# Performance work log

Hardware: AMD Instinct MI355X
Metric: run time of the kernel (lower is better)

## Reference

```python
import jax, jax.numpy as jnp
import numpy as np


def setup_inputs() -> dict:
    key = jax.random.key(0)
    ks = jax.random.split(key, 4)
    B, T, D, U = 64, 512, 1024, 1024
    scale = 1.0 / np.sqrt(D)
    return {
        "x": jax.random.normal(ks[0], (B, T, D), dtype=jnp.float32),
        "kernel_z": jax.random.normal(ks[1], (D, U), dtype=jnp.float32) * scale,
        "kernel_r": jax.random.normal(ks[2], (D, U), dtype=jnp.float32) * scale,
        "kernel_h": jax.random.normal(ks[3], (D, U), dtype=jnp.float32) * scale,
        "memory_z": jnp.ones((U,), dtype=jnp.float32),
        "memory_r": jnp.ones((U,), dtype=jnp.float32),
        "bias_z": jnp.zeros((U,), dtype=jnp.float32),
        "bias_r": jnp.zeros((U,), dtype=jnp.float32),
        "bias_h": jnp.zeros((U,), dtype=jnp.float32),
    }


def _bru_scan(x, kernel_z, kernel_r, kernel_h, memory_z, memory_r,
              bias_z, bias_r, bias_h):
    B, T, D = x.shape
    U = kernel_z.shape[1]
    # Precompute the three input projections for all timesteps at once
    # (same math as per-step K.dot; hoisted out of the recurrence).
    xz = jnp.einsum('btd,du->btu', x, kernel_z) + bias_z  # [B,T,U]
    xr = jnp.einsum('btd,du->btu', x, kernel_r) + bias_r
    xh = jnp.einsum('btd,du->btu', x, kernel_h) + bias_h

    def step(h, xs):
        xz_t, xr_t, xh_t = xs
        r = jnp.tanh(xr_t + h * memory_r) + 1.0
        z = jax.nn.sigmoid(xz_t + h * memory_z)
        hh = jnp.tanh(xh_t + r * h)
        out = (1.0 - z) * hh + z * h
        return out, out

    h0 = jnp.zeros((B, U), dtype=x.dtype)
    # scan over time axis
    xs = (jnp.swapaxes(xz, 0, 1), jnp.swapaxes(xr, 0, 1), jnp.swapaxes(xh, 0, 1))
    _, outs = jax.lax.scan(step, h0, xs)  # outs: [T,B,U]
    return jnp.swapaxes(outs, 0, 1)  # [B,T,U]


def reference(x, kernel_z, kernel_r, kernel_h, memory_z, memory_r,
              bias_z, bias_r, bias_h):
    return _bru_scan(x, kernel_z, kernel_r, kernel_h, memory_z, memory_r,
                     bias_z, bias_r, bias_h)
```

## Files before the change

kernel.cpp:

```cpp
#include <hip/hip_runtime.h>
#include <cmath>

using f16x8 = __attribute__((ext_vector_type(8))) _Float16;
using f32x4 = __attribute__((ext_vector_type(4))) float;

__device__ __forceinline__ void gld16(void* lds, const void* g) {
    __builtin_amdgcn_global_load_lds(
        (const __attribute__((address_space(1))) unsigned int*)g,
        (__attribute__((address_space(3))) unsigned int*)lds, 16, 0, 0);
}


__global__ __launch_bounds__(256)
void bru_conv_a(const float* __restrict__ x, char* __restrict__ Ablob,
                int T, int D, int Tc, int t0, int Mc)
{
    const int gid = blockIdx.x * 256 + threadIdx.x;
    const int kt = gid / Mc;
    const int m  = gid - kt * Mc;
    const int mt = m >> 7, row = m & 127;

    const long xrow = (long)(m / Tc) * T + t0 + (m % Tc);
    const float* src = x + xrow * (long)D + kt * 32;

    float v[32];
    #pragma unroll
    for (int i = 0; i < 8; ++i)
        *(float4*)&v[i * 4] = *(const float4*)(src + i * 4);

    _Float16 hi[32], lo[32];
    #pragma unroll
    for (int k = 0; k < 32; ++k) {
        hi[k] = (_Float16)v[k];
        lo[k] = (_Float16)(v[k] - (float)hi[k]);
    }

    char* base = Ablob + ((size_t)(mt * 34 + kt)) * 16384 + (size_t)row * 128;
    #pragma unroll
    for (int q = 0; q < 4; ++q) {
        _Float16 oh[8], ol[8];
        #pragma unroll
        for (int j = 0; j < 8; ++j) { oh[j] = hi[q * 8 + j]; ol[j] = lo[q * 8 + j]; }
        *(f16x8*)(base + (((q    ) ^ (row & 7)) << 4)) = *(f16x8*)oh;
        *(f16x8*)(base + (((q + 4) ^ (row & 7)) << 4)) = *(f16x8*)ol;
    }
}

__global__ __launch_bounds__(256)
void bru_conv_w(const float* __restrict__ wz, const float* __restrict__ wr,
                const float* __restrict__ wh, char* __restrict__ Wblob,
                int D, int U)
{
    const int gid  = blockIdx.x * 256 + threadIdx.x;
    const int blob = gid >> 8;
    const int row  = gid & 255;

    const int g    = blob >> 7;
    const int rest = blob & 127;
    const int nt   = rest >> 5;
    const int kt   = rest & 31;

    const float* W = (g == 0) ? wz : (g == 1) ? wr : wh;
    const int ucol = nt * 256 + row;

    char* base = Wblob + ((size_t)((g * 4 + nt) * 34 + kt)) * 16384 + (size_t)row * 64;
    #pragma unroll
    for (int q = 0; q < 4; ++q) {
        _Float16 o[8];
        #pragma unroll
        for (int j = 0; j < 8; ++j)
            o[j] = (_Float16)W[(long)(kt * 32 + q * 8 + j) * U + ucol];
        *(f16x8*)(base + ((q ^ ((row >> 1) & 3)) << 4)) = *(f16x8*)o;
    }
}

__global__ __launch_bounds__(256, 2)
void bru_gemm_mfma(const char* __restrict__ Ablob, const char* __restrict__ Wblob,
                   const float* __restrict__ bz, const float* __restrict__ br,
                   const float* __restrict__ bh,
                   _Float16* __restrict__ proj,
                   int nmt, int U, int Mc)
{
    __shared__ char sm[65536];

    const int ngrid = gridDim.x;
    const int bid   = blockIdx.x;
    int lid = bid;
    if ((ngrid & 7) == 0) lid = (bid & 7) * (ngrid >> 3) + (bid >> 3);
    const int mt  = lid / 12;
    const int rem = lid - mt * 12;
    const int g   = rem >> 2;
    const int nt  = rem & 3;

    const int tid  = threadIdx.x;
    const int lane = tid & 63;
    const int w    = tid >> 6;
    const int wm   = w >> 1, wn = w & 1;
    const int l15  = lane & 15;
    const int lgrp = lane >> 4;

    const char* asrc = Ablob + (size_t)(mt * 34) * 16384;
    const char* bsrc = Wblob + (size_t)((g * 4 + nt) * 34) * 16384;
    const int st = tid * 16;

    const int abase = (wm * 64 + l15) * 128;
    const int slotA = (lgrp ^ (l15 & 7)) << 4;
    const int bbase = 32768 + (wn * 128 + l15) * 64;
    const int slotB = (lgrp ^ ((l15 >> 1) & 3)) << 4;

    f32x4 acc[4][8];
    #pragma unroll
    for (int i = 0; i < 4; ++i)
        #pragma unroll
        for (int j = 0; j < 8; ++j) acc[i][j] = (f32x4)0.f;

#define STAGE(kt_) do { \
    const int bb_ = (kt_) & 1; \
    _Pragma("unroll") for (int c_ = 0; c_ < 4; ++c_) \
        gld16(sm + bb_ * 16384 + c_ * 4096 + st, \
              asrc + (size_t)(kt_) * 16384 + c_ * 4096 + st); \
    _Pragma("unroll") for (int c_ = 0; c_ < 4; ++c_) \
        gld16(sm + 32768 + bb_ * 16384 + c_ * 4096 + st, \
              bsrc + (size_t)(kt_) * 16384 + c_ * 4096 + st); } while (0)

    STAGE(0);
    __syncthreads();

    for (int kt = 0; kt < 32; ++kt) {
        STAGE(kt + 1);

        const char* sa = sm + (kt & 1) * 16384;
        const char* sb = sm + (kt & 1) * 16384;

        f16x8 bf[8];
        #pragma unroll
        for (int j = 0; j < 8; ++j)
            bf[j] = *(const f16x8*)(sb + bbase + j * 1024 + slotB);
        #pragma unroll
        for (int f = 0; f < 4; ++f) {
            f16x8 ah = *(const f16x8*)(sa + abase + f * 2048 + slotA);
            f16x8 al = *(const f16x8*)(sa + abase + f * 2048 + (slotA ^ 64));
            #pragma unroll
            for (int j = 0; j < 8; ++j) {
                acc[f][j] = __builtin_amdgcn_mfma_f32_16x16x32_f16(ah, bf[j], acc[f][j], 0, 0, 0);
                acc[f][j] = __builtin_amdgcn_mfma_f32_16x16x32_f16(al, bf[j], acc[f][j], 0, 0, 0);
            }
        }

        __syncthreads();
    }
#undef STAGE

    const float* bias = (g == 0) ? bz : (g == 1) ? br : bh;
    const int n0 = nt * 256 + wn * 128;
    float bcol[8];
    #pragma unroll
    for (int j = 0; j < 8; ++j) bcol[j] = bias[n0 + j * 16 + l15];

    _Float16* cbase = proj + (size_t)g * Mc * U + (size_t)n0 + l15;
    #pragma unroll
    for (int f = 0; f < 4; ++f) {
        #pragma unroll
        for (int reg = 0; reg < 4; ++reg) {
            const int row = mt * 128 + wm * 64 + f * 16 + lgrp * 4 + reg;
            #pragma unroll
            for (int j = 0; j < 8; ++j)
                cbase[(size_t)row * U + j * 16] = (_Float16)(acc[f][j][reg] + bcol[j]);
        }
    }
}

#define PF 8
__global__ __launch_bounds__(256)
void bru_scan(const _Float16* __restrict__ proj,
              const float* __restrict__ mz, const float* __restrict__ mr,
              float* __restrict__ out,
              float* __restrict__ hstate,
              int B, int T, int U, int Tc, int t0, int Mc)
{
    const int idx = blockIdx.x * blockDim.x + threadIdx.x;
    const int b = idx / U;
    const int u = idx - b * U;

    float h = (t0 == 0) ? 0.f : hstate[idx];
    const float vmz = mz[u];
    const float vmr = mr[u];

    const _Float16* pz = proj + (long)b * Tc * U + u;
    const _Float16* pr = pz + (long)Mc * U;
    const _Float16* ph = pr + (long)Mc * U;
    float* po = out + ((long)b * T + t0) * U + u;

    _Float16 fz[PF], fr[PF], fh[PF];
    #pragma unroll
    for (int i = 0; i < PF; ++i) {
        const long o = (long)((i < Tc) ? i : (Tc - 1)) * U;
        fz[i] = pz[o]; fr[i] = pr[o]; fh[i] = ph[o];
    }

    for (int t = 0; t < Tc; t += PF) {
        #pragma unroll
        for (int i = 0; i < PF; ++i) {
            const float xz = (float)fz[i];
            const float xr = (float)fr[i];
            const float xh = (float)fh[i];
            {
                int tn = t + i + PF; if (tn > Tc - 1) tn = Tc - 1;
                const long o = (long)tn * U;
                fz[i] = pz[o]; fr[i] = pr[o]; fh[i] = ph[o];
            }
            const float e2r = __expf(2.f * (xr + h * vmr));
            const float rr  = 2.f - 2.f / (e2r + 1.f);
            const float zz  = 1.f / (1.f + __expf(-(xz + h * vmz)));
            const float e2h = __expf(2.f * (xh + rr * h));
            const float hh  = 1.f - 2.f / (e2h + 1.f);
            h = (1.f - zz) * hh + zz * h;
            if (t + i < Tc) po[(long)(t + i) * U] = h;
        }
    }
    hstate[idx] = h;
}

extern "C" void kernel_launch(void* const* d_in, const int* in_sizes, int n_in,
                              void* d_out, int out_size, void* d_ws, size_t ws_size,
                              hipStream_t stream)
{
    const float* x  = (const float*)d_in[0];
    const float* wz = (const float*)d_in[1];
    const float* wr = (const float*)d_in[2];
    const float* wh = (const float*)d_in[3];
    const float* mz = (const float*)d_in[4];
    const float* mr = (const float*)d_in[5];
    const float* bz = (const float*)d_in[6];
    const float* br = (const float*)d_in[7];
    const float* bh = (const float*)d_in[8];

    const int B = 64, T = 512, D = 1024, U = 1024;

    const size_t h_bytes = (size_t)B * U * sizeof(float);
    const size_t w_bytes = (size_t)12 * 34 * 16384;

    int Tc = T;
    while (Tc > 4) {
        const int nmt_ = B * Tc / 128;
        const size_t a_bytes_ = (size_t)nmt_ * 34 * 16384;
        const size_t p_bytes_ = 3ull * B * Tc * U * sizeof(_Float16);
        if (h_bytes + w_bytes + a_bytes_ + p_bytes_ <= ws_size) break;
        Tc >>= 1;
    }
    const int nmt = B * Tc / 128;
    const int Mc  = B * Tc;
    const size_t a_bytes = (size_t)nmt * 34 * 16384;

    float*    h_state = (float*)d_ws;
    char*     Wblob   = (char*)d_ws + h_bytes;
    char*     Ablob   = (char*)d_ws + h_bytes + w_bytes;
    _Float16* proj    = (_Float16*)((char*)d_ws + h_bytes + w_bytes + a_bytes);

    bru_conv_w<<<12 * 32 * 256 / 256, 256, 0, stream>>>(wz, wr, wh, Wblob, D, U);

    for (int t0 = 0; t0 < T; t0 += Tc) {
        bru_conv_a<<<(Mc * 32) / 256, 256, 0, stream>>>(x, Ablob, T, D, Tc, t0, Mc);

        bru_gemm_mfma<<<3 * nmt * 4, 256, 0, stream>>>(
            Ablob, Wblob, bz, br, bh, proj, nmt, U, Mc);

        bru_scan<<<(B * U) / 256, 256, 0, stream>>>(
            proj, mz, mr, (float*)d_out, h_state, B, T, U, Tc, t0, Mc);
    }
}
```

Before: 541.9 us.

## Load GEMM B operand directly from global into registers, halve LDS

The weight matrix is repacked into an MFMA-fragment-ordered layout so each lane fetches its B fragments straight from global/L2 into registers, double-buffered across k-steps. LDS use drops to 32KB and holds only the A tiles, which removes the LDS staging and reads for B. In exchange each block issues many more global loads per k-step, since B is no longer shared through LDS, and keeps 16 extra vector registers live, which may hurt occupancy or latency hiding. The weight conversion kernel is rewritten to emit the new layout.

Result: no change. 543.0 us (+0.2%).

```diff
diff --git a/kernel.cpp b/kernel.cpp
--- a/kernel.cpp
+++ b/kernel.cpp
@@ -51,27 +51,20 @@
                 const float* __restrict__ wh, char* __restrict__ Wblob,
                 int D, int U)
 {
-    const int gid  = blockIdx.x * 256 + threadIdx.x;
-    const int blob = gid >> 8;
-    const int row  = gid & 255;
-
-    const int g    = blob >> 7;
-    const int rest = blob & 127;
-    const int nt   = rest >> 5;
-    const int kt   = rest & 31;
+    const int gid = blockIdx.x * 256 + threadIdx.x;
+    const int g    = gid >> 17;
+    const int rest = gid & 131071;
+    const int qg   = rest >> 10;
+    const int u    = rest & 1023;
 
     const float* W = (g == 0) ? wz : (g == 1) ? wr : wh;
-    const int ucol = nt * 256 + row;
-
-    char* base = Wblob + ((size_t)((g * 4 + nt) * 34 + kt)) * 16384 + (size_t)row * 64;
-    #pragma unroll
-    for (int q = 0; q < 4; ++q) {
-        _Float16 o[8];
-        #pragma unroll
-        for (int j = 0; j < 8; ++j)
-            o[j] = (_Float16)W[(long)(kt * 32 + q * 8 + j) * U + ucol];
-        *(f16x8*)(base + ((q ^ ((row >> 1) & 3)) << 4)) = *(f16x8*)o;
-    }
+
+    _Float16 o[8];
+    #pragma unroll
+    for (int e = 0; e < 8; ++e)
+        o[e] = (_Float16)W[(long)(qg * 8 + e) * U + u];
+
+    *(f16x8*)(Wblob + (((size_t)(g * 136 + qg) << 10) + u) * 16) = *(f16x8*)o;
 }
 
 __global__ __launch_bounds__(256, 2)
@@ -81,7 +74,7 @@
                    _Float16* __restrict__ proj,
                    int nmt, int U, int Mc)
 {
-    __shared__ char sm[65536];
+    __shared__ char sm[32768];
 
     const int ngrid = gridDim.x;
     const int bid   = blockIdx.x;
@@ -100,13 +93,13 @@
     const int lgrp = lane >> 4;
 
     const char* asrc = Ablob + (size_t)(mt * 34) * 16384;
-    const char* bsrc = Wblob + (size_t)((g * 4 + nt) * 34) * 16384;
     const int st = tid * 16;
 
     const int abase = (wm * 64 + l15) * 128;
     const int slotA = (lgrp ^ (l15 & 7)) << 4;
-    const int bbase = 32768 + (wn * 128 + l15) * 64;
-    const int slotB = (lgrp ^ ((l15 >> 1) & 3)) << 4;
+
+    const char* bptr = Wblob + (((size_t)(g * 136) << 10)
+                                + (size_t)(nt * 256 + wn * 128 + l15)) * 16;
 
     f32x4 acc[4][8];
     #pragma unroll
@@ -114,42 +107,48 @@
         #pragma unroll
         for (int j = 0; j < 8; ++j) acc[i][j] = (f32x4)0.f;
 
-#define STAGE(kt_) do { \
-    const int bb_ = (kt_) & 1; \
+    f16x8 Be[8], Bo[8];
+
+#define STAGE_A(kt_, buf_) \
     _Pragma("unroll") for (int c_ = 0; c_ < 4; ++c_) \
-        gld16(sm + bb_ * 16384 + c_ * 4096 + st, \
-              asrc + (size_t)(kt_) * 16384 + c_ * 4096 + st); \
-    _Pragma("unroll") for (int c_ = 0; c_ < 4; ++c_) \
-        gld16(sm + 32768 + bb_ * 16384 + c_ * 4096 + st, \
-              bsrc + (size_t)(kt_) * 16384 + c_ * 4096 + st); } while (0)
-
-    STAGE(0);
+        gld16(sm + (buf_) * 16384 + c_ * 4096 + st, \
+              asrc + (size_t)(kt_) * 16384 + c_ * 4096 + st);
+
+#define LOADB(dst, kt_) \
+    _Pragma("unroll") for (int j_ = 0; j_ < 8; ++j_) \
+        dst[j_] = *(const f16x8*)(bptr + ((((size_t)((kt_) * 4 + lgrp)) << 10) \
+                                          + (size_t)(j_ * 16)) * 16);
+
+#define COMPUTE(buf_, BB) do { \
+    const char* sa_ = sm + (buf_) * 16384; \
+    _Pragma("unroll") for (int f_ = 0; f_ < 4; ++f_) { \
+        f16x8 ah_ = *(const f16x8*)(sa_ + abase + f_ * 2048 + slotA); \
+        f16x8 al_ = *(const f16x8*)(sa_ + abase + f_ * 2048 + (slotA ^ 64)); \
+        _Pragma("unroll") for (int j_ = 0; j_ < 8; ++j_) { \
+            acc[f_][j_] = __builtin_amdgcn_mfma_f32_16x16x32_f16(ah_, BB[j_], acc[f_][j_], 0, 0, 0); \
+            acc[f_][j_] = __builtin_amdgcn_mfma_f32_16x16x32_f16(al_, BB[j_], acc[f_][j_], 0, 0, 0); } } \
+    } while (0)
+
+    STAGE_A(0, 0);
+    LOADB(Be, 0);
     __syncthreads();
 
-    for (int kt = 0; kt < 32; ++kt) {
-        STAGE(kt + 1);
-
-        const char* sa = sm + (kt & 1) * 16384;
-        const char* sb = sm + (kt & 1) * 16384;
-
-        f16x8 bf[8];
-        #pragma unroll
-        for (int j = 0; j < 8; ++j)
-            bf[j] = *(const f16x8*)(sb + bbase + j * 1024 + slotB);
-        #pragma unroll
-        for (int f = 0; f < 4; ++f) {
-            f16x8 ah = *(const f16x8*)(sa + abase + f * 2048 + slotA);
-            f16x8 al = *(const f16x8*)(sa + abase + f * 2048 + (slotA ^ 64));
-            #pragma unroll
-            for (int j = 0; j < 8; ++j) {
-                acc[f][j] = __builtin_amdgcn_mfma_f32_16x16x32_f16(ah, bf[j], acc[f][j], 0, 0, 0);
-                acc[f][j] = __builtin_amdgcn_mfma_f32_16x16x32_f16(al, bf[j], acc[f][j], 0, 0, 0);
-            }
-        }
-
+    for (int kt2 = 0; kt2 < 16; ++kt2) {
+        const int kt = 2 * kt2;
+
+        STAGE_A(kt + 1, 1);
+        LOADB(Bo, kt + 1);
+        COMPUTE(0, Be);
         __syncthreads();
-    }
-#undef STAGE
+
+        STAGE_A(kt + 2, 0);
+        LOADB(Be, kt + 2);
+        COMPUTE(1, Bo);
+        __syncthreads();
+    }
+#undef STAGE_A
+#undef LOADB
+#undef COMPUTE
 
     const float* bias = (g == 0) ? bz : (g == 1) ? br : bh;
     const int n0 = nt * 256 + wn * 128;
@@ -238,7 +237,7 @@
     const int B = 64, T = 512, D = 1024, U = 1024;
 
     const size_t h_bytes = (size_t)B * U * sizeof(float);
-    const size_t w_bytes = (size_t)12 * 34 * 16384;
+    const size_t w_bytes = (size_t)3 * 136 * 1024 * 16;
 
     int Tc = T;
     while (Tc > 4) {
@@ -257,7 +256,7 @@
     char*     Ablob   = (char*)d_ws + h_bytes + w_bytes;
     _Float16* proj    = (_Float16*)((char*)d_ws + h_bytes + w_bytes + a_bytes);
 
-    bru_conv_w<<<12 * 32 * 256 / 256, 256, 0, stream>>>(wz, wr, wh, Wblob, D, U);
+    bru_conv_w<<<3 * 128 * 1024 / 256, 256, 0, stream>>>(wz, wr, wh, Wblob, D, U);
 
     for (int t0 = 0; t0 < T; t0 += Tc) {
         bru_conv_a<<<(Mc * 32) / 256, 256, 0, stream>>>(x, Ablob, T, D, Tc, t0, Mc);
```
